# Optimization experiments

Measured on AMD Instinct MI355X. Metric: run time of the kernel, lower is better.

Reference implementation:

```python
import jax, jax.numpy as jnp
import numpy as np

B, D_IN, H0, H1, LAT, C = 8192, 2048, 1024, 512, 128, 8
SCALE = 0.02  # weight init scale to keep activations well-conditioned


def _unshared_linear_relu(x, labels, W, b):
    """Per-cluster Linear+ReLU routing. x:[B,din], W:[C,din,dout], b:[C,dout].
    Computes all cluster branches then selects per-row branch (same math as
    torch's mask gather->Linear->scatter; rows never reorder)."""
    y = jax.nn.relu(jnp.einsum('bi,cio->bco', x, W) + b[None, :, :])  # [B,C,dout]
    return jnp.take_along_axis(y, labels[:, None, None], axis=1)[:, 0, :]


def setup_inputs() -> dict:
    key = jax.random.key(0)
    ks = jax.random.split(key, 12)
    return {
        'x': jax.random.normal(ks[0], (B, D_IN), dtype=jnp.float32),
        'cluster_labels': jax.random.randint(ks[1], (B,), 0, C, dtype=jnp.int32),
        'eps': jax.random.normal(ks[2], (B, LAT), dtype=jnp.float32),
        'W_enc0': jax.random.normal(ks[3], (C, D_IN, H0), dtype=jnp.float32) * SCALE,
        'b_enc0': jnp.zeros((C, H0), dtype=jnp.float32),
        'W_enc1': jax.random.normal(ks[4], (H0, H1), dtype=jnp.float32) * SCALE,
        'b_enc1': jnp.zeros((H1,), dtype=jnp.float32),
        'W_mu': jax.random.normal(ks[5], (H1, LAT), dtype=jnp.float32) * SCALE,
        'b_mu': jnp.zeros((LAT,), dtype=jnp.float32),
        'W_logvar': jax.random.normal(ks[6], (H1, LAT), dtype=jnp.float32) * SCALE,
        'b_logvar': jnp.zeros((LAT,), dtype=jnp.float32),
        'W_dec0': jax.random.normal(ks[7], (LAT, H1), dtype=jnp.float32) * SCALE,
        'b_dec0': jnp.zeros((H1,), dtype=jnp.float32),
        'W_dec1': jax.random.normal(ks[8], (C, H1, H0), dtype=jnp.float32) * SCALE,
        'b_dec1': jnp.zeros((C, H0), dtype=jnp.float32),
        'W_out': jax.random.normal(ks[9], (H0, D_IN), dtype=jnp.float32) * SCALE,
        'b_out': jnp.zeros((D_IN,), dtype=jnp.float32),
    }


def reference(x, cluster_labels, eps,
              W_enc0, b_enc0, W_enc1, b_enc1,
              W_mu, b_mu, W_logvar, b_logvar,
              W_dec0, b_dec0, W_dec1, b_dec1,
              W_out, b_out):
    labels = cluster_labels.astype(jnp.int32)
    # encoder: unshared layer 0, shared layer 1
    h = _unshared_linear_relu(x, labels, W_enc0, b_enc0)          # [B, H0]
    h = jax.nn.relu(h @ W_enc1 + b_enc1)                          # [B, H1]
    # shared latent heads
    mu = h @ W_mu + b_mu                                          # [B, LAT]
    logvar = h @ W_logvar + b_logvar                              # [B, LAT]
    # reparameterize
    z = mu + eps * jnp.exp(0.5 * logvar)                          # [B, LAT]
    # decoder: shared layer 0, unshared layer 1 (hidden_dims reversed)
    d = jax.nn.relu(z @ W_dec0 + b_dec0)                          # [B, H1]
    d = _unshared_linear_relu(d, labels, W_dec1, b_dec1)          # [B, H0]
    # shared output layer (no activation)
    recon = d @ W_out + b_out                                     # [B, D_IN]
    return recon, mu, logvar
```

## Files before the change

### kernel.cpp

```cpp
#include <hip/hip_runtime.h>


#define DEVI __device__ __forceinline__

constexpr int B_    = 8192;
constexpr int DIN   = 2048;
constexpr int H0_   = 1024;
constexpr int H1_   = 512;
constexpr int LAT_  = 128;
constexpr int NC    = 8;

constexpr int BM = 128, BN = 128, BK = 32;
constexpr int TCAP   = 72;
constexpr int BP_CAP = TCAP * BM;

#define MI_NTILES 8
#define MI_TILEC  16

typedef __attribute__((ext_vector_type(8))) short bf16x8;
typedef __attribute__((ext_vector_type(4))) float f32x4;

#define VMBAR(N) asm volatile("s_waitcnt vmcnt(" #N ") lgkmcnt(0)\n\ts_barrier" ::: "memory")

DEVI unsigned short f2bf(float f) {
  union { float f; unsigned u; } a; a.f = f;
  unsigned r = a.u + 0x7fffu + ((a.u >> 16) & 1u);
  return (unsigned short)(r >> 16);
}

DEVI void glds16(const unsigned short* g, unsigned short* l) {
  __builtin_amdgcn_global_load_lds(
      (const __attribute__((address_space(1))) unsigned int*)g,
      (__attribute__((address_space(3))) unsigned int*)l,
      16, 0, 0);
}

constexpr size_t AL256(size_t x) { return (x + 255) & ~(size_t)255; }
constexpr size_t OFF_META = 0;
constexpr size_t OFF_PERM = 512;
constexpr size_t OFF_XG   = AL256(OFF_PERM + (size_t)BP_CAP * 4);
constexpr size_t OFF_H0   = AL256(OFF_XG  + (size_t)BP_CAP * DIN * 2);
constexpr size_t OFF_H1   = AL256(OFF_H0  + (size_t)BP_CAP * H0_ * 2);
constexpr size_t OFF_MLP  = AL256(OFF_H1  + (size_t)BP_CAP * H1_ * 2);
constexpr size_t OFF_BML  = AL256(OFF_MLP + (size_t)BP_CAP * 256 * 4);
constexpr size_t OFF_WT0  = AL256(OFF_BML + 256 * 4);
constexpr size_t OFF_WT1  = AL256(OFF_WT0 + (size_t)NC * DIN * H0_ * 2);
constexpr size_t OFF_WML  = AL256(OFF_WT1 + (size_t)H0_ * H1_ * 2);
constexpr size_t OFF_WD0  = AL256(OFF_WML + (size_t)256 * H1_ * 2);
constexpr size_t OFF_WD1  = AL256(OFF_WD0 + (size_t)LAT_ * H1_ * 2);
constexpr size_t OFF_WOUT = AL256(OFF_WD1 + (size_t)NC * H1_ * H0_ * 2);

__global__ void setup_all(const int* __restrict__ labels, int* __restrict__ meta,
                          int* __restrict__ perm, const float* __restrict__ b_mu,
                          const float* __restrict__ b_lv, float* __restrict__ b_ml) {
  __shared__ int cnt[NC], base[NC];
  int t = threadIdx.x;
  if (t < NC) cnt[t] = 0;
  if (t < 256) b_ml[t] = (t < 128) ? b_mu[t] : b_lv[t - 128];
  __syncthreads();
  for (int i = t; i < B_; i += 1024) atomicAdd(&cnt[labels[i]], 1);
  for (int i = t; i < BP_CAP; i += 1024) perm[i] = -1;
  __syncthreads();
  if (t == 0) {
    int off = 0, nt = 0;
    for (int c = 0; c < NC; ++c) {
      base[c] = off;
      int k = (cnt[c] + BM - 1) >> 7;
      for (int j = 0; j < k; ++j) meta[MI_TILEC + nt + j] = c;
      nt += k;
      off += k << 7;
    }
    meta[MI_NTILES] = nt;
  }
  __syncthreads();
  if (t < NC) cnt[t] = base[t];
  __syncthreads();
  for (int i = t; i < B_; i += 1024) {
    int pos = atomicAdd(&cnt[labels[i]], 1);
    perm[pos] = i;
  }
}

struct SegDesc { const float* src; unsigned short* dst; int K, N, nb, tstart; };
struct SegTable { SegDesc s[7]; };

__global__ void convert_all(SegTable t) {
  __shared__ float tl[64][33];
  int tile = blockIdx.x;
  int si = 0;
#pragma unroll
  for (int i = 1; i < 7; ++i) si += (tile >= t.s[i].tstart) ? 1 : 0;
  const SegDesc sd = t.s[si];
  int local = tile - sd.tstart;
  int tpb = (sd.K >> 6) * (sd.N >> 5);
  int b = local / tpb, rem = local - b * tpb;
  int tk = rem / (sd.N >> 5), tn = rem - tk * (sd.N >> 5);
  const float* s = sd.src + (size_t)b * sd.K * sd.N;
  unsigned short* d = sd.dst + (size_t)b * sd.K * sd.N;
  int n0 = tn * 32, k0 = tk * 64;
  int tx = threadIdx.x, ty = threadIdx.y;
  for (int i = ty; i < 64; i += 8)
    tl[i][tx] = s[(size_t)(k0 + i) * sd.N + n0 + tx];
  __syncthreads();
  int id = ty * 32 + tx;
  int j = id >> 3;
  int kk = (id & 7) * 8;
  unsigned short v[8];
#pragma unroll
  for (int q = 0; q < 8; ++q) v[q] = f2bf(tl[kk + q][j]);
  *(int4*)&d[(size_t)(n0 + j) * sd.K + k0 + kk] = *(int4*)v;
}

__global__ void gather_x_kernel(const float* __restrict__ x, const int* __restrict__ perm,
                                unsigned short* __restrict__ xg) {
  int p = blockIdx.x;
  int c4 = blockIdx.y * 256 + threadIdx.x;
  int src = perm[p];
  float4 v = make_float4(0.f, 0.f, 0.f, 0.f);
  if (src >= 0) v = ((const float4*)(x + (size_t)src * DIN))[c4];
  ushort4 o;
  o.x = f2bf(v.x); o.y = f2bf(v.y); o.z = f2bf(v.z); o.w = f2bf(v.w);
  ((ushort4*)(xg + (size_t)p * DIN))[c4] = o;
}

__global__ void z_kernel(const float* __restrict__ mlp, const float* __restrict__ eps,
                         const int* __restrict__ perm, unsigned short* __restrict__ z,
                         float* __restrict__ out_mu, float* __restrict__ out_lv) {
  int p = blockIdx.x, j = threadIdx.x;
  int src = perm[p];
  float zz = 0.f;
  if (src >= 0) {
    float m = mlp[(size_t)p * 256 + j];
    float l = mlp[(size_t)p * 256 + 128 + j];
    zz = m + eps[(size_t)src * LAT_ + j] * expf(0.5f * l);
    out_mu[(size_t)src * LAT_ + j] = m;
    out_lv[(size_t)src * LAT_ + j] = l;
  }
  z[(size_t)p * LAT_ + j] = f2bf(zz);
}

template <int OUT_MODE, bool RELU, bool PCW, bool PCB>
__global__ __launch_bounds__(256, 2)
void gemm_kernel(const unsigned short* __restrict__ A,
                 const unsigned short* __restrict__ Bt,
                 const float* __restrict__ bias,
                 void* __restrict__ Cout,
                 const int* __restrict__ meta,
                 const int* __restrict__ perm,
                 int K, int N, int ldc) {
  const int ntn = N >> 7;
  const int sup = 8 * ntn;
  const int gid = blockIdx.x;
  const int tm  = (gid / sup) * 8 + (gid & 7);
  const int tn  = (gid % sup) >> 3;
  if (tm >= meta[MI_NTILES]) return;

  int cluster = 0;
  if (PCW || PCB) cluster = meta[MI_TILEC + tm];
  const unsigned short* Bp = Bt + (PCW ? (size_t)cluster * (size_t)N * K : 0);
  const float* bb = bias + (PCB ? (size_t)cluster * N : 0);

  __shared__ alignas(16) unsigned short As[3][BM * BK];
  __shared__ alignas(16) unsigned short Bs[3][BN * BK];

  const int tid  = threadIdx.x;
  const int w    = tid >> 6, lane = tid & 63;
  const int fr   = lane & 15, quad = lane >> 4;
  const int wm   = (w >> 1) * 64, wn = (w & 1) * 64;

  const int sU = (w * 2 + 0) * 64 + lane;
  const int sV = (w * 2 + 1) * 64 + lane;
  const int rU = sU >> 2, rV = sV >> 2;
  const int cU = (sU & 3) ^ ((rU >> 1) & 3);
  const int cV = (sV & 3) ^ ((rV >> 1) & 3);
  const unsigned short* paU = A  + (size_t)(tm * BM + rU) * K + cU * 8;
  const unsigned short* paV = A  + (size_t)(tm * BM + rV) * K + cV * 8;
  const unsigned short* pbU = Bp + (size_t)(tn * BN + rU) * K + cU * 8;
  const unsigned short* pbV = Bp + (size_t)(tn * BN + rV) * K + cV * 8;
  const int ldU = (w * 2 + 0) * 512;
  const int ldV = (w * 2 + 1) * 512;

  int aro[4], bro[4];
#pragma unroll
  for (int i = 0; i < 4; ++i) {
    int R = wm + i * 16 + fr;
    aro[i] = (R * 4 + (quad ^ ((R >> 1) & 3))) * 8;
    R = wn + i * 16 + fr;
    bro[i] = (R * 4 + (quad ^ ((R >> 1) & 3))) * 8;
  }

  f32x4 acc[4][4] = {};

  auto stage = [&](int buf, int k0) {
    glds16(paU + k0, &As[buf][ldU]);
    glds16(paV + k0, &As[buf][ldV]);
    glds16(pbU + k0, &Bs[buf][ldU]);
    glds16(pbV + k0, &Bs[buf][ldV]);
  };

  auto compute = [&](int buf) {
    bf16x8 af[4], bfr[4];
#pragma unroll
    for (int i = 0; i < 4; ++i) af[i]  = *(const bf16x8*)&As[buf][aro[i]];
#pragma unroll
    for (int i = 0; i < 4; ++i) bfr[i] = *(const bf16x8*)&Bs[buf][bro[i]];
#pragma unroll
    for (int mi = 0; mi < 4; ++mi)
#pragma unroll
      for (int ni = 0; ni < 4; ++ni)
        acc[mi][ni] = __builtin_amdgcn_mfma_f32_16x16x32_bf16(af[mi], bfr[ni], acc[mi][ni], 0, 0, 0);
  };

  const int nt = K / BK;

  stage(0, 0);
  stage(1, BK);
  VMBAR(4);

  int cur = 0;
  for (int i = 0; i < nt; ++i) {
    if (i + 2 < nt) {
      int b2 = cur + 2; if (b2 >= 3) b2 -= 3;
      stage(b2, (i + 2) * BK);
    }
    compute(cur);
    if (i + 2 < nt)      VMBAR(4);
    else if (i + 1 < nt) VMBAR(0);
    ++cur; if (cur == 3) cur = 0;
  }

  float bv[4];
#pragma unroll
  for (int ni = 0; ni < 4; ++ni) bv[ni] = bb[tn * BN + wn + ni * 16 + fr];

#pragma unroll
  for (int mi = 0; mi < 4; ++mi) {
#pragma unroll
    for (int r = 0; r < 4; ++r) {
      int m = tm * BM + wm + mi * 16 + quad * 4 + r;
      int orow = m;
      if (OUT_MODE == 2) orow = perm[m];
#pragma unroll
      for (int ni = 0; ni < 4; ++ni) {
        int n = tn * BN + wn + ni * 16 + fr;
        float v = acc[mi][ni][r] + bv[ni];
        if (RELU) v = fmaxf(v, 0.f);
        if (OUT_MODE == 0) {
          ((unsigned short*)Cout)[(size_t)m * N + n] = f2bf(v);
        } else if (OUT_MODE == 1) {
          ((float*)Cout)[(size_t)m * N + n] = v;
        } else {
          if (orow >= 0) ((float*)Cout)[(size_t)orow * ldc + n] = v;
        }
      }
    }
  }
}

extern "C" void kernel_launch(void* const* d_in, const int* in_sizes, int n_in,
                              void* d_out, int out_size, void* d_ws, size_t ws_size,
                              hipStream_t stream) {
  const float* x        = (const float*)d_in[0];
  const int*   labels   = (const int*)d_in[1];
  const float* eps      = (const float*)d_in[2];
  const float* W_enc0   = (const float*)d_in[3];
  const float* b_enc0   = (const float*)d_in[4];
  const float* W_enc1   = (const float*)d_in[5];
  const float* b_enc1   = (const float*)d_in[6];
  const float* W_mu     = (const float*)d_in[7];
  const float* b_mu     = (const float*)d_in[8];
  const float* W_logvar = (const float*)d_in[9];
  const float* b_logvar = (const float*)d_in[10];
  const float* W_dec0   = (const float*)d_in[11];
  const float* b_dec0   = (const float*)d_in[12];
  const float* W_dec1   = (const float*)d_in[13];
  const float* b_dec1   = (const float*)d_in[14];
  const float* W_out    = (const float*)d_in[15];
  const float* b_out    = (const float*)d_in[16];

  float* out_recon = (float*)d_out;
  float* out_mu    = out_recon + (size_t)B_ * DIN;
  float* out_lv    = out_mu + (size_t)B_ * LAT_;

  char* ws = (char*)d_ws;
  int* meta            = (int*)(ws + OFF_META);
  int* perm            = (int*)(ws + OFF_PERM);
  unsigned short* xg   = (unsigned short*)(ws + OFF_XG);
  unsigned short* h0   = (unsigned short*)(ws + OFF_H0);
  unsigned short* h1   = (unsigned short*)(ws + OFF_H1);
  float* mlp           = (float*)(ws + OFF_MLP);
  float* b_ml          = (float*)(ws + OFF_BML);
  unsigned short* Wt0  = (unsigned short*)(ws + OFF_WT0);
  unsigned short* Wt1  = (unsigned short*)(ws + OFF_WT1);
  unsigned short* Wml  = (unsigned short*)(ws + OFF_WML);
  unsigned short* Wd0  = (unsigned short*)(ws + OFF_WD0);
  unsigned short* Wd1  = (unsigned short*)(ws + OFF_WD1);
  unsigned short* Wout = (unsigned short*)(ws + OFF_WOUT);
  unsigned short* d1 = xg;
  unsigned short* d0 = h0;
  unsigned short* z  = h1;

  SegTable st;
  int ts = 0;
  auto seg = [&](int i, const float* s, unsigned short* d, int K, int N, int nb) {
    st.s[i] = SegDesc{s, d, K, N, nb, ts};
    ts += (K / 64) * (N / 32) * nb;
  };
  seg(0, W_enc0,   Wt0,                      DIN,  H0_,  NC);
  seg(1, W_enc1,   Wt1,                      H0_,  H1_,  1);
  seg(2, W_mu,     Wml,                      H1_,  LAT_, 1);
  seg(3, W_logvar, Wml + (size_t)LAT_ * H1_, H1_,  LAT_, 1);
  seg(4, W_dec0,   Wd0,                      LAT_, H1_,  1);
  seg(5, W_dec1,   Wd1,                      H1_,  H0_,  NC);
  seg(6, W_out,    Wout,                     H0_,  DIN,  1);

  setup_all<<<1, 1024, 0, stream>>>(labels, meta, perm, b_mu, b_logvar, b_ml);
  convert_all<<<ts, dim3(32, 8), 0, stream>>>(st);
  gather_x_kernel<<<dim3(BP_CAP, DIN / (256 * 4)), 256, 0, stream>>>(x, perm, xg);

  gemm_kernel<0, true, true, true><<<TCAP * (H0_ / BN), 256, 0, stream>>>(
      xg, Wt0, b_enc0, h0, meta, perm, DIN, H0_, 0);
  gemm_kernel<0, true, false, false><<<TCAP * (H1_ / BN), 256, 0, stream>>>(
      h0, Wt1, b_enc1, h1, meta, perm, H0_, H1_, 0);
  gemm_kernel<1, false, false, false><<<TCAP * (256 / BN), 256, 0, stream>>>(
      h1, Wml, b_ml, mlp, meta, perm, H1_, 256, 0);
  z_kernel<<<BP_CAP, 128, 0, stream>>>(mlp, eps, perm, z, out_mu, out_lv);
  gemm_kernel<0, true, false, false><<<TCAP * (H1_ / BN), 256, 0, stream>>>(
      z, Wd0, b_dec0, d0, meta, perm, LAT_, H1_, 0);
  gemm_kernel<0, true, true, true><<<TCAP * (H0_ / BN), 256, 0, stream>>>(
      d0, Wd1, b_dec1, d1, meta, perm, H1_, H0_, 0);
  gemm_kernel<2, false, false, false><<<TCAP * (DIN / BN), 256, 0, stream>>>(
      d1, Wout, b_out, out_recon, meta, perm, H0_, DIN, DIN);

  (void)in_sizes; (void)n_in; (void)out_size; (void)ws_size;
}
```

Before: 438.7 us.

## Switch GEMM pipeline to double-buffered 64-deep K stages

Replaces the three-stage BK=32 ring buffer with a two-stage double buffer where each stage loads two BK=32 sub-tiles (an effective K step of 64). This halves the number of barriers and waitcnt points per K loop and issues more loads per stage. In exchange, prefetch depth drops to a single stage and the wait now drains all outstanding loads (vmcnt 0), which may expose more memory latency. LDS use grows from 3 to 4 tile slots.

```diff
diff --git a/kernel.cpp b/kernel.cpp
--- a/kernel.cpp
+++ b/kernel.cpp
@@ -11,6 +11,7 @@
 constexpr int NC    = 8;
 
 constexpr int BM = 128, BN = 128, BK = 32;
+constexpr int DK = 64;
 constexpr int TCAP   = 72;
 constexpr int BP_CAP = TCAP * BM;
 
@@ -20,7 +21,7 @@
 typedef __attribute__((ext_vector_type(8))) short bf16x8;
 typedef __attribute__((ext_vector_type(4))) float f32x4;
 
-#define VMBAR(N) asm volatile("s_waitcnt vmcnt(" #N ") lgkmcnt(0)\n\ts_barrier" ::: "memory")
+#define VMBAR0() asm volatile("s_waitcnt vmcnt(0) lgkmcnt(0)\n\ts_barrier" ::: "memory")
 
 DEVI unsigned short f2bf(float f) {
   union { float f; unsigned u; } a; a.f = f;
@@ -160,8 +161,8 @@
   const unsigned short* Bp = Bt + (PCW ? (size_t)cluster * (size_t)N * K : 0);
   const float* bb = bias + (PCB ? (size_t)cluster * N : 0);
 
-  __shared__ alignas(16) unsigned short As[3][BM * BK];
-  __shared__ alignas(16) unsigned short Bs[3][BN * BK];
+  __shared__ alignas(16) unsigned short As[2][2][BM * BK];
+  __shared__ alignas(16) unsigned short Bs[2][2][BN * BK];
 
   const int tid  = threadIdx.x;
   const int w    = tid >> 6, lane = tid & 63;
@@ -192,41 +193,43 @@
   f32x4 acc[4][4] = {};
 
   auto stage = [&](int buf, int k0) {
-    glds16(paU + k0, &As[buf][ldU]);
-    glds16(paV + k0, &As[buf][ldV]);
-    glds16(pbU + k0, &Bs[buf][ldU]);
-    glds16(pbV + k0, &Bs[buf][ldV]);
+    glds16(paU + k0, &As[buf][0][ldU]);
+    glds16(paV + k0, &As[buf][0][ldV]);
+    glds16(pbU + k0, &Bs[buf][0][ldU]);
+    glds16(pbV + k0, &Bs[buf][0][ldV]);
+    glds16(paU + k0 + BK, &As[buf][1][ldU]);
+    glds16(paV + k0 + BK, &As[buf][1][ldV]);
+    glds16(pbU + k0 + BK, &Bs[buf][1][ldU]);
+    glds16(pbV + k0 + BK, &Bs[buf][1][ldV]);
   };
 
   auto compute = [&](int buf) {
-    bf16x8 af[4], bfr[4];
-#pragma unroll
-    for (int i = 0; i < 4; ++i) af[i]  = *(const bf16x8*)&As[buf][aro[i]];
-#pragma unroll
-    for (int i = 0; i < 4; ++i) bfr[i] = *(const bf16x8*)&Bs[buf][bro[i]];
-#pragma unroll
-    for (int mi = 0; mi < 4; ++mi)
-#pragma unroll
-      for (int ni = 0; ni < 4; ++ni)
-        acc[mi][ni] = __builtin_amdgcn_mfma_f32_16x16x32_bf16(af[mi], bfr[ni], acc[mi][ni], 0, 0, 0);
+#pragma unroll
+    for (int sub = 0; sub < 2; ++sub) {
+      bf16x8 af[4], bfr[4];
+#pragma unroll
+      for (int i = 0; i < 4; ++i) af[i]  = *(const bf16x8*)&As[buf][sub][aro[i]];
+#pragma unroll
+      for (int i = 0; i < 4; ++i) bfr[i] = *(const bf16x8*)&Bs[buf][sub][bro[i]];
+#pragma unroll
+      for (int mi = 0; mi < 4; ++mi)
+#pragma unroll
+        for (int ni = 0; ni < 4; ++ni)
+          acc[mi][ni] = __builtin_amdgcn_mfma_f32_16x16x32_bf16(af[mi], bfr[ni], acc[mi][ni], 0, 0, 0);
+    }
   };
 
-  const int nt = K / BK;
+  const int ndp = K / DK;
 
   stage(0, 0);
-  stage(1, BK);
-  VMBAR(4);
+  VMBAR0();
 
   int cur = 0;
-  for (int i = 0; i < nt; ++i) {
-    if (i + 2 < nt) {
-      int b2 = cur + 2; if (b2 >= 3) b2 -= 3;
-      stage(b2, (i + 2) * BK);
-    }
+  for (int i = 0; i < ndp; ++i) {
+    if (i + 1 < ndp) stage(cur ^ 1, (i + 1) * DK);
     compute(cur);
-    if (i + 2 < nt)      VMBAR(4);
-    else if (i + 1 < nt) VMBAR(0);
-    ++cur; if (cur == 3) cur = 0;
+    if (i + 1 < ndp) VMBAR0();
+    cur ^= 1;
   }
 
   float bv[4];
```

Result: slower. 456.3 us (+4.0%).
